# Performance work log

Hardware: AMD Instinct MI355X
Metric: run time of the kernel (lower is better)

The kernel has to match this reference:

```python
import jax, jax.numpy as jnp
import numpy as np
import math

N_HEADS = 8

def setup_inputs() -> dict:
    key = jax.random.key(0)
    ks = jax.random.split(key, 5)
    B, S, D = 2, 4096, 512
    return {
        "x": jax.random.normal(ks[0], (B, S, D), jnp.float32),
        "W_in": jax.random.normal(ks[1], (D, 3 * D), jnp.float32) * (1.0 / math.sqrt(D)),
        "b_in": jax.random.normal(ks[2], (3 * D,), jnp.float32) * 0.02,
        "W_out": jax.random.normal(ks[3], (D, D), jnp.float32) * (1.0 / math.sqrt(D)),
        "b_out": jax.random.normal(ks[4], (D,), jnp.float32) * 0.02,
        "causal_mask": 1,
    }

def reference(x, W_in, b_in, W_out, b_out, causal_mask):
    B, S, D = x.shape
    H = N_HEADS
    dh = D // H
    qkv = x @ W_in + b_in                      # [B,S,3D]
    q, k, v = jnp.split(qkv, 3, axis=-1)
    # [B,S,D] -> [B,H,S,dh]
    q = q.reshape(B, S, H, dh).transpose(0, 2, 1, 3)
    k = k.reshape(B, S, H, dh).transpose(0, 2, 1, 3)
    v = v.reshape(B, S, H, dh).transpose(0, 2, 1, 3)
    scores = jnp.einsum("bhqd,bhkd->bhqk", q, k)  # [B,H,S,S]
    if causal_mask:
        # strictly upper triangle masked to -inf (before scaling, as in torch code)
        causal = jnp.tril(jnp.ones((S, S), dtype=bool))
        scores = jnp.where(causal, scores, -jnp.inf)
    scores = scores / math.sqrt(dh)
    w = jax.nn.softmax(scores, axis=-1)
    out = jnp.einsum("bhqk,bhkd->bhqd", w, v)     # [B,H,S,dh]
    out = out.transpose(0, 2, 1, 3).reshape(B, S, D)
    return out @ W_out + b_out
```

## Files before the change

kernel.cpp:

```cpp
#include <hip/hip_runtime.h>
#include <stdint.h>

typedef __attribute__((ext_vector_type(8))) short bf16x8;
typedef __attribute__((ext_vector_type(4))) float f32x4;

__device__ __forceinline__ float bf2f(unsigned short b) {
  union { unsigned int u; float f; } c; c.u = ((unsigned int)b) << 16; return c.f;
}
__device__ __forceinline__ unsigned short f2bf(float f) {
  union { float f; unsigned int u; } c; c.f = f;
  unsigned int u = c.u;
  return (unsigned short)((u + 0x7fffu + ((u >> 16) & 1u)) >> 16);
}

__device__ __forceinline__ void gload_lds16(const void* g, void* l) {
  __builtin_amdgcn_global_load_lds((const __attribute__((address_space(1))) void*)g,
                                   (__attribute__((address_space(3))) void*)l,
                                   16, 0, 0);
}


__global__ __launch_bounds__(256) void cvt_x(const float* __restrict__ in,
                                             unsigned short* __restrict__ out, int n4) {
  int i = blockIdx.x * 256 + threadIdx.x;
  if (i < n4) {
    float4 f = ((const float4*)in)[i];
    ushort4 o;
    o.x = f2bf(f.x); o.y = f2bf(f.y); o.z = f2bf(f.z); o.w = f2bf(f.w);
    ((ushort4*)out)[i] = o;
  }
}

__global__ __launch_bounds__(256) void tw_cvt(const float* __restrict__ W,
                                              unsigned short* __restrict__ Wt, int N) {
  int idx = blockIdx.x * 256 + threadIdx.x;
  int n = idx >> 9, k = idx & 511;
  Wt[idx] = f2bf(W[(size_t)k * N + n]);
}


template<int QKV>
__global__ __launch_bounds__(256)
void gemm_bt(const unsigned short* __restrict__ A, const unsigned short* __restrict__ Bt,
             const float* __restrict__ bias, float* __restrict__ Cout,
             unsigned short* __restrict__ qo, unsigned short* __restrict__ ko,
             unsigned short* __restrict__ vo, int M, int N, int K) {
  __shared__ unsigned short As[128 * 64];
  __shared__ unsigned short Bs[128 * 64];
  const int tid = threadIdx.x;
  const int wid = tid >> 6;
  const int lane = tid & 63;
  const int row0 = blockIdx.x * 128;
  const int col0 = blockIdx.y * 128;

  f32x4 acc[4][4];
#pragma unroll
  for (int m = 0; m < 4; ++m)
#pragma unroll
    for (int n = 0; n < 4; ++n)
      acc[m][n] = (f32x4){0.f, 0.f, 0.f, 0.f};

  const int wr = (wid >> 1) * 64;
  const int wc = (wid & 1) * 64;
  const int rw = lane & 15;
  const int nk = K >> 6;

  for (int kt = 0; kt < nk; ++kt) {
    const int k0 = kt << 6;
#pragma unroll
    for (int i = 0; i < 4; ++i) {
      int c = i * 256 + tid;
      int r = c >> 3, kq = (c & 7) << 3;
      gload_lds16(A + (size_t)(row0 + r) * K + k0 + kq, As + (size_t)(i * 256 + wid * 64) * 8);
    }
#pragma unroll
    for (int i = 0; i < 4; ++i) {
      int c = i * 256 + tid;
      int r = c >> 3, kq = (c & 7) << 3;
      gload_lds16(Bt + (size_t)(col0 + r) * K + k0 + kq, Bs + (size_t)(i * 256 + wid * 64) * 8);
    }
    __syncthreads();
#pragma unroll
    for (int ks = 0; ks < 2; ++ks) {
      const int kof = ks * 32 + (lane >> 4) * 8;
      bf16x8 af[4], bfr[4];
#pragma unroll
      for (int m = 0; m < 4; ++m)
        af[m] = *(const bf16x8*)&As[(wr + m * 16 + rw) * 64 + kof];
#pragma unroll
      for (int n = 0; n < 4; ++n)
        bfr[n] = *(const bf16x8*)&Bs[(wc + n * 16 + rw) * 64 + kof];
#pragma unroll
      for (int m = 0; m < 4; ++m)
#pragma unroll
        for (int n = 0; n < 4; ++n)
          acc[m][n] = __builtin_amdgcn_mfma_f32_16x16x32_bf16(af[m], bfr[n], acc[m][n], 0, 0, 0);
    }
    __syncthreads();
  }

  const int lr4 = (lane >> 4) * 4;
  const int lc = lane & 15;
#pragma unroll
  for (int m = 0; m < 4; ++m) {
#pragma unroll
    for (int n = 0; n < 4; ++n) {
      const int col = col0 + wc + n * 16 + lc;
      const float bb = bias[col];
      const int row = row0 + wr + m * 16 + lr4;
      if (QKV) {
        const int which = col >> 9;
        const int rem = col & 511, h = rem >> 6, d = rem & 63;
        const int b = row >> 12, s = row & 4095;
        if (which == 2) {
          ushort4 u;
          u.x = f2bf(acc[m][n][0] + bb);
          u.y = f2bf(acc[m][n][1] + bb);
          u.z = f2bf(acc[m][n][2] + bb);
          u.w = f2bf(acc[m][n][3] + bb);
          *(ushort4*)&vo[(((size_t)(b * 8 + h) * 64 + d) << 12) + s] = u;
        } else {
          const float scale = (which == 0) ? 0.125f : 1.0f;
          unsigned short* dst = (which == 0) ? qo : ko;
#pragma unroll
          for (int r2 = 0; r2 < 4; ++r2)
            dst[(((size_t)(b * 8 + h) * 4096 + (s + r2)) << 6) + d] =
                f2bf((acc[m][n][r2] + bb) * scale);
        }
      } else {
#pragma unroll
        for (int r2 = 0; r2 < 4; ++r2)
          Cout[(size_t)(row + r2) * N + col] = acc[m][n][r2] + bb;
      }
    }
  }
}


__global__ __launch_bounds__(512, 2)
void attn_mfma(const unsigned short* __restrict__ Qb, const unsigned short* __restrict__ Kb,
               const unsigned short* __restrict__ Vtb, unsigned short* __restrict__ Ob,
               const int* __restrict__ causal_p) {
  __shared__ unsigned short Qs[256 * 64];
  __shared__ unsigned short Ks[64 * 64];
  __shared__ unsigned short Vs[64 * 64];
  __shared__ unsigned short Ps[8][32 * 64];

  const int tid = threadIdx.x;
  const int wid = tid >> 6;
  const int lane = tid & 63;
  const int lx = lane & 15, ly = lane >> 4, l7 = lane & 7;
  const int p = blockIdx.x;
  const int bh = blockIdx.y;
  const int causal = *causal_p;
  const int qtile = (wid < 4) ? p : (31 - p);
  const int qw = qtile * 128 + (wid & 3) * 32;
  const int qldsb = ((wid < 4) ? 0 : 128) + (wid & 3) * 32;
  const size_t qkbase = (size_t)bh * 4096 * 64;
  const size_t vbase = (size_t)bh * 64 * 4096;

  {
    const int pa = p, pb = 31 - p;
#pragma unroll
    for (int i = 0; i < 4; ++i) {
      int c = i * 512 + tid;
      int r = c >> 3, ch = c & 7;
      int qrow = (r < 128) ? (pa * 128 + r) : (pb * 128 + (r - 128));
      gload_lds16(Qb + qkbase + (size_t)qrow * 64 + ((ch ^ (r & 7)) << 3),
                  Qs + (size_t)(i * 512 + wid * 64) * 8);
    }
  }

  f32x4 o[2][4];
  float mrow[2][4], lrow[2][4];
#pragma unroll
  for (int rf = 0; rf < 2; ++rf) {
#pragma unroll
    for (int df = 0; df < 4; ++df) o[rf][df] = (f32x4){0.f, 0.f, 0.f, 0.f};
#pragma unroll
    for (int r = 0; r < 4; ++r) { mrow[rf][r] = -1e30f; lrow[rf][r] = 0.f; }
  }

  const int ktmax = causal ? (63 - 2 * p) : 63;
  for (int kt = 0; kt <= ktmax; ++kt) {
    __syncthreads();
    {
      int r = tid >> 3, ch = tid & 7;
      gload_lds16(Kb + qkbase + (size_t)(kt * 64 + r) * 64 + ((ch ^ (r & 7)) << 3),
                  Ks + (size_t)(wid * 64) * 8);
      gload_lds16(Vtb + vbase + (size_t)r * 4096 + kt * 64 + ((ch ^ (r & 7)) << 3),
                  Vs + (size_t)(wid * 64) * 8);
    }
    __syncthreads();

    const int ktb = kt * 64;
    if (!causal || ktb <= qw + 31) {
      f32x4 s[2][4];
#pragma unroll
      for (int rf = 0; rf < 2; ++rf)
#pragma unroll
        for (int cf = 0; cf < 4; ++cf) s[rf][cf] = (f32x4){0.f, 0.f, 0.f, 0.f};
#pragma unroll
      for (int ks = 0; ks < 2; ++ks) {
        const int kel = ((ks * 4 + ly) ^ l7) << 3;
        bf16x8 a[2], bb[4];
#pragma unroll
        for (int rf = 0; rf < 2; ++rf)
          a[rf] = *(const bf16x8*)&Qs[(qldsb + rf * 16 + lx) * 64 + kel];
#pragma unroll
        for (int cf = 0; cf < 4; ++cf)
          bb[cf] = *(const bf16x8*)&Ks[(cf * 16 + lx) * 64 + kel];
#pragma unroll
        for (int rf = 0; rf < 2; ++rf)
#pragma unroll
          for (int cf = 0; cf < 4; ++cf)
            s[rf][cf] = __builtin_amdgcn_mfma_f32_16x16x32_bf16(a[rf], bb[cf], s[rf][cf], 0, 0, 0);
      }

      const bool diag = causal && (ktb + 63 > qw);
#pragma unroll
      for (int rf = 0; rf < 2; ++rf) {
#pragma unroll
        for (int r = 0; r < 4; ++r) {
          const int qg = qw + rf * 16 + ly * 4 + r;
          if (diag) {
#pragma unroll
            for (int cf = 0; cf < 4; ++cf)
              if (ktb + cf * 16 + lx > qg) s[rf][cf][r] = -1e30f;
          }
          float tm = fmaxf(fmaxf(s[rf][0][r], s[rf][1][r]), fmaxf(s[rf][2][r], s[rf][3][r]));
          tm = fmaxf(tm, __shfl_xor(tm, 1));
          tm = fmaxf(tm, __shfl_xor(tm, 2));
          tm = fmaxf(tm, __shfl_xor(tm, 4));
          tm = fmaxf(tm, __shfl_xor(tm, 8));
          const float mo = mrow[rf][r];
          const float mn = fmaxf(mo, tm);
          const float scl = __expf(mo - mn);
          float ls = 0.f;
          const int ql = rf * 16 + ly * 4 + r;
          const int swz = (ql & 7) << 3;
#pragma unroll
          for (int cf = 0; cf < 4; ++cf) {
            float pv = __expf(s[rf][cf][r] - mn);
            ls += pv;
            Ps[wid][ql * 64 + ((cf * 16 + lx) ^ swz)] = f2bf(pv);
          }
          ls += __shfl_xor(ls, 1);
          ls += __shfl_xor(ls, 2);
          ls += __shfl_xor(ls, 4);
          ls += __shfl_xor(ls, 8);
          lrow[rf][r] = lrow[rf][r] * scl + ls;
          mrow[rf][r] = mn;
#pragma unroll
          for (int df = 0; df < 4; ++df) o[rf][df][r] *= scl;
        }
      }

#pragma unroll
      for (int ks = 0; ks < 2; ++ks) {
        const int kel = ((ks * 4 + ly) ^ l7) << 3;
        bf16x8 pa[2], vb_[4];
#pragma unroll
        for (int rf = 0; rf < 2; ++rf)
          pa[rf] = *(const bf16x8*)&Ps[wid][(rf * 16 + lx) * 64 + kel];
#pragma unroll
        for (int df = 0; df < 4; ++df)
          vb_[df] = *(const bf16x8*)&Vs[(df * 16 + lx) * 64 + kel];
#pragma unroll
        for (int rf = 0; rf < 2; ++rf)
#pragma unroll
          for (int df = 0; df < 4; ++df)
            o[rf][df] = __builtin_amdgcn_mfma_f32_16x16x32_bf16(pa[rf], vb_[df], o[rf][df], 0, 0, 0);
      }
    }
  }

  const int b = bh >> 3, h = bh & 7;
#pragma unroll
  for (int rf = 0; rf < 2; ++rf) {
#pragma unroll
    for (int r = 0; r < 4; ++r) {
      const float inv = 1.0f / lrow[rf][r];
      const int row = b * 4096 + qw + rf * 16 + ly * 4 + r;
#pragma unroll
      for (int df = 0; df < 4; ++df)
        Ob[(size_t)row * 512 + h * 64 + df * 16 + lx] = f2bf(o[rf][df][r] * inv);
    }
  }
}


extern "C" void kernel_launch(void* const* d_in, const int* in_sizes, int n_in,
                              void* d_out, int out_size, void* d_ws, size_t ws_size,
                              hipStream_t stream) {
  const float* x     = (const float*)d_in[0];
  const float* W_in  = (const float*)d_in[1];
  const float* b_in  = (const float*)d_in[2];
  const float* W_out = (const float*)d_in[3];
  const float* b_out = (const float*)d_in[4];
  const int* causal  = (const int*)d_in[5];
  float* out = (float*)d_out;

  unsigned short* xb   = (unsigned short*)d_ws;
  unsigned short* wint = xb + 4194304;
  unsigned short* wout = wint + 786432;
  unsigned short* qb   = wout + 262144;
  unsigned short* kb   = qb + 4194304;
  unsigned short* vt   = kb + 4194304;

  cvt_x<<<4096, 256, 0, stream>>>(x, xb, 4194304 / 4);
  tw_cvt<<<3072, 256, 0, stream>>>(W_in, wint, 1536);
  tw_cvt<<<1024, 256, 0, stream>>>(W_out, wout, 512);

  gemm_bt<1><<<dim3(64, 12), 256, 0, stream>>>(xb, wint, b_in, nullptr, qb, kb, vt,
                                               8192, 1536, 512);

  attn_mfma<<<dim3(16, 16), 512, 0, stream>>>(qb, kb, vt, xb, causal);

  gemm_bt<0><<<dim3(64, 4), 256, 0, stream>>>(xb, wout, b_out, out, nullptr, nullptr, nullptr,
                                              8192, 512, 512);
}
```

Measured before the change: 347.9 us.

## Restructure attention with double-buffered K/V, register Q, lazy softmax rescale

The attention kernel moves to 256-thread blocks, one query tile each and launched largest-first. It keeps Q fragments in registers and double-buffers K/V tiles in LDS so the next tile's load overlaps compute. Softmax now works in base 2, with log2e folded into the Q scale. It skips the max reduction and rescale when the running max stays within a threshold, and defers the row-sum shuffles to the end. Separately, the weight transpose-convert now goes through LDS tiles, and V is written row-major and then transposed by a new kernel through the output buffer, which adds a launch and extra traffic.

```diff
diff --git a/kernel.cpp b/kernel.cpp
--- a/kernel.cpp
+++ b/kernel.cpp
@@ -18,6 +18,8 @@
                                    (__attribute__((address_space(3))) void*)l,
                                    16, 0, 0);
 }
+
+#define QSCALE 0.18033688011112042f
 
 
 __global__ __launch_bounds__(256) void cvt_x(const float* __restrict__ in,
@@ -31,11 +33,44 @@
   }
 }
 
-__global__ __launch_bounds__(256) void tw_cvt(const float* __restrict__ W,
-                                              unsigned short* __restrict__ Wt, int N) {
-  int idx = blockIdx.x * 256 + threadIdx.x;
-  int n = idx >> 9, k = idx & 511;
-  Wt[idx] = f2bf(W[(size_t)k * N + n]);
+__global__ __launch_bounds__(256)
+void tw_cvt_t(const float* __restrict__ W, unsigned short* __restrict__ Wt, int N) {
+  __shared__ unsigned short T[64][68];
+  const int n0 = blockIdx.x * 64, k0 = blockIdx.y * 64;
+  const int c = threadIdx.x & 15, r = threadIdx.x >> 4;
+#pragma unroll
+  for (int i = 0; i < 4; ++i) {
+    float4 f = *(const float4*)&W[(size_t)(k0 + i * 16 + r) * N + n0 + c * 4];
+    T[c * 4 + 0][i * 16 + r] = f2bf(f.x);
+    T[c * 4 + 1][i * 16 + r] = f2bf(f.y);
+    T[c * 4 + 2][i * 16 + r] = f2bf(f.z);
+    T[c * 4 + 3][i * 16 + r] = f2bf(f.w);
+  }
+  __syncthreads();
+#pragma unroll
+  for (int i = 0; i < 4; ++i)
+    *(ushort4*)&Wt[(size_t)(n0 + i * 16 + r) * 512 + k0 + c * 4] =
+        *(const ushort4*)&T[i * 16 + r][c * 4];
+}
+
+__global__ __launch_bounds__(256)
+void vtr(const unsigned short* __restrict__ vsd, unsigned short* __restrict__ vt) {
+  __shared__ unsigned short T[64][68];
+  const int bh = blockIdx.y, s0 = blockIdx.x * 64;
+  const int c = threadIdx.x & 15, r = threadIdx.x >> 4;
+#pragma unroll
+  for (int i = 0; i < 4; ++i) {
+    ushort4 u = *(const ushort4*)&vsd[((size_t)bh * 4096 + s0 + i * 16 + r) * 64 + c * 4];
+    T[c * 4 + 0][i * 16 + r] = u.x;
+    T[c * 4 + 1][i * 16 + r] = u.y;
+    T[c * 4 + 2][i * 16 + r] = u.z;
+    T[c * 4 + 3][i * 16 + r] = u.w;
+  }
+  __syncthreads();
+#pragma unroll
+  for (int i = 0; i < 4; ++i)
+    *(ushort4*)&vt[((size_t)bh * 64 + i * 16 + r) * 4096 + s0 + c * 4] =
+        *(const ushort4*)&T[i * 16 + r][c * 4];
 }
 
 
@@ -112,21 +147,12 @@
         const int which = col >> 9;
         const int rem = col & 511, h = rem >> 6, d = rem & 63;
         const int b = row >> 12, s = row & 4095;
-        if (which == 2) {
-          ushort4 u;
-          u.x = f2bf(acc[m][n][0] + bb);
-          u.y = f2bf(acc[m][n][1] + bb);
-          u.z = f2bf(acc[m][n][2] + bb);
-          u.w = f2bf(acc[m][n][3] + bb);
-          *(ushort4*)&vo[(((size_t)(b * 8 + h) * 64 + d) << 12) + s] = u;
-        } else {
-          const float scale = (which == 0) ? 0.125f : 1.0f;
-          unsigned short* dst = (which == 0) ? qo : ko;
-#pragma unroll
-          for (int r2 = 0; r2 < 4; ++r2)
-            dst[(((size_t)(b * 8 + h) * 4096 + (s + r2)) << 6) + d] =
-                f2bf((acc[m][n][r2] + bb) * scale);
-        }
+        const float scale = (which == 0) ? QSCALE : 1.0f;
+        unsigned short* dst = (which == 0) ? qo : ((which == 1) ? ko : vo);
+#pragma unroll
+        for (int r2 = 0; r2 < 4; ++r2)
+          dst[(((size_t)(b * 8 + h) * 4096 + (s + r2)) << 6) + d] =
+              f2bf((acc[m][n][r2] + bb) * scale);
       } else {
 #pragma unroll
         for (int r2 = 0; r2 < 4; ++r2)
@@ -137,61 +163,70 @@
 }
 
 
-__global__ __launch_bounds__(512, 2)
+__global__ __launch_bounds__(256, 3)
 void attn_mfma(const unsigned short* __restrict__ Qb, const unsigned short* __restrict__ Kb,
                const unsigned short* __restrict__ Vtb, unsigned short* __restrict__ Ob,
                const int* __restrict__ causal_p) {
-  __shared__ unsigned short Qs[256 * 64];
-  __shared__ unsigned short Ks[64 * 64];
-  __shared__ unsigned short Vs[64 * 64];
-  __shared__ unsigned short Ps[8][32 * 64];
+  __shared__ unsigned short Ks[2][64 * 64];
+  __shared__ unsigned short Vs[2][64 * 64];
+  __shared__ unsigned short Ps[4][32 * 64];
 
   const int tid = threadIdx.x;
   const int wid = tid >> 6;
   const int lane = tid & 63;
   const int lx = lane & 15, ly = lane >> 4, l7 = lane & 7;
-  const int p = blockIdx.x;
+  const int p = 31 - blockIdx.x;
   const int bh = blockIdx.y;
   const int causal = *causal_p;
-  const int qtile = (wid < 4) ? p : (31 - p);
-  const int qw = qtile * 128 + (wid & 3) * 32;
-  const int qldsb = ((wid < 4) ? 0 : 128) + (wid & 3) * 32;
+  const int qw = p * 128 + wid * 32;
   const size_t qkbase = (size_t)bh * 4096 * 64;
   const size_t vbase = (size_t)bh * 64 * 4096;
 
-  {
-    const int pa = p, pb = 31 - p;
-#pragma unroll
-    for (int i = 0; i < 4; ++i) {
-      int c = i * 512 + tid;
-      int r = c >> 3, ch = c & 7;
-      int qrow = (r < 128) ? (pa * 128 + r) : (pb * 128 + (r - 128));
-      gload_lds16(Qb + qkbase + (size_t)qrow * 64 + ((ch ^ (r & 7)) << 3),
-                  Qs + (size_t)(i * 512 + wid * 64) * 8);
-    }
-  }
+  bf16x8 qf[2][2];
+#pragma unroll
+  for (int rf = 0; rf < 2; ++rf)
+#pragma unroll
+    for (int ks = 0; ks < 2; ++ks)
+      qf[rf][ks] =
+          *(const bf16x8*)(Qb + qkbase + (size_t)(qw + rf * 16 + lx) * 64 + ks * 32 + ly * 8);
 
   f32x4 o[2][4];
-  float mrow[2][4], lrow[2][4];
+  float mrow[2][4], lpart[2][4];
 #pragma unroll
   for (int rf = 0; rf < 2; ++rf) {
 #pragma unroll
     for (int df = 0; df < 4; ++df) o[rf][df] = (f32x4){0.f, 0.f, 0.f, 0.f};
 #pragma unroll
-    for (int r = 0; r < 4; ++r) { mrow[rf][r] = -1e30f; lrow[rf][r] = 0.f; }
-  }
-
-  const int ktmax = causal ? (63 - 2 * p) : 63;
+    for (int r = 0; r < 4; ++r) { mrow[rf][r] = -1e30f; lpart[rf][r] = 0.f; }
+  }
+
+  const int ktmax = causal ? (2 * p + 1) : 63;
+
+#pragma unroll
+  for (int pass = 0; pass < 2; ++pass) {
+    int c = pass * 256 + tid;
+    int r = c >> 3, ch = c & 7;
+    gload_lds16(Kb + qkbase + (size_t)r * 64 + ((ch ^ (r & 7)) << 3),
+                &Ks[0][(size_t)(pass * 256 + wid * 64) * 8]);
+    gload_lds16(Vtb + vbase + (size_t)r * 4096 + ((ch ^ (r & 7)) << 3),
+                &Vs[0][(size_t)(pass * 256 + wid * 64) * 8]);
+  }
+  __syncthreads();
+
+  int cur = 0;
   for (int kt = 0; kt <= ktmax; ++kt) {
-    __syncthreads();
-    {
-      int r = tid >> 3, ch = tid & 7;
-      gload_lds16(Kb + qkbase + (size_t)(kt * 64 + r) * 64 + ((ch ^ (r & 7)) << 3),
-                  Ks + (size_t)(wid * 64) * 8);
-      gload_lds16(Vtb + vbase + (size_t)r * 4096 + kt * 64 + ((ch ^ (r & 7)) << 3),
-                  Vs + (size_t)(wid * 64) * 8);
-    }
-    __syncthreads();
+    if (kt < ktmax) {
+      const int nx = kt + 1;
+#pragma unroll
+      for (int pass = 0; pass < 2; ++pass) {
+        int c = pass * 256 + tid;
+        int r = c >> 3, ch = c & 7;
+        gload_lds16(Kb + qkbase + (size_t)(nx * 64 + r) * 64 + ((ch ^ (r & 7)) << 3),
+                    &Ks[cur ^ 1][(size_t)(pass * 256 + wid * 64) * 8]);
+        gload_lds16(Vtb + vbase + (size_t)r * 4096 + nx * 64 + ((ch ^ (r & 7)) << 3),
+                    &Vs[cur ^ 1][(size_t)(pass * 256 + wid * 64) * 8]);
+      }
+    }
 
     const int ktb = kt * 64;
     if (!causal || ktb <= qw + 31) {
@@ -203,76 +238,104 @@
 #pragma unroll
       for (int ks = 0; ks < 2; ++ks) {
         const int kel = ((ks * 4 + ly) ^ l7) << 3;
-        bf16x8 a[2], bb[4];
+        bf16x8 kf[4];
+#pragma unroll
+        for (int cf = 0; cf < 4; ++cf)
+          kf[cf] = *(const bf16x8*)&Ks[cur][(cf * 16 + lx) * 64 + kel];
 #pragma unroll
         for (int rf = 0; rf < 2; ++rf)
-          a[rf] = *(const bf16x8*)&Qs[(qldsb + rf * 16 + lx) * 64 + kel];
-#pragma unroll
-        for (int cf = 0; cf < 4; ++cf)
-          bb[cf] = *(const bf16x8*)&Ks[(cf * 16 + lx) * 64 + kel];
-#pragma unroll
-        for (int rf = 0; rf < 2; ++rf)
 #pragma unroll
           for (int cf = 0; cf < 4; ++cf)
-            s[rf][cf] = __builtin_amdgcn_mfma_f32_16x16x32_bf16(a[rf], bb[cf], s[rf][cf], 0, 0, 0);
+            s[rf][cf] = __builtin_amdgcn_mfma_f32_16x16x32_bf16(qf[rf][ks], kf[cf], s[rf][cf], 0, 0, 0);
       }
 
       const bool diag = causal && (ktb + 63 > qw);
+      float tmx[2][4];
+      bool ok = true;
 #pragma unroll
       for (int rf = 0; rf < 2; ++rf) {
 #pragma unroll
         for (int r = 0; r < 4; ++r) {
-          const int qg = qw + rf * 16 + ly * 4 + r;
           if (diag) {
+            const int qg = qw + rf * 16 + ly * 4 + r;
 #pragma unroll
             for (int cf = 0; cf < 4; ++cf)
               if (ktb + cf * 16 + lx > qg) s[rf][cf][r] = -1e30f;
           }
-          float tm = fmaxf(fmaxf(s[rf][0][r], s[rf][1][r]), fmaxf(s[rf][2][r], s[rf][3][r]));
-          tm = fmaxf(tm, __shfl_xor(tm, 1));
-          tm = fmaxf(tm, __shfl_xor(tm, 2));
-          tm = fmaxf(tm, __shfl_xor(tm, 4));
-          tm = fmaxf(tm, __shfl_xor(tm, 8));
-          const float mo = mrow[rf][r];
-          const float mn = fmaxf(mo, tm);
-          const float scl = __expf(mo - mn);
-          float ls = 0.f;
-          const int ql = rf * 16 + ly * 4 + r;
-          const int swz = (ql & 7) << 3;
-#pragma unroll
-          for (int cf = 0; cf < 4; ++cf) {
-            float pv = __expf(s[rf][cf][r] - mn);
-            ls += pv;
-            Ps[wid][ql * 64 + ((cf * 16 + lx) ^ swz)] = f2bf(pv);
+          const float a0 = fmaxf(s[rf][0][r], s[rf][1][r]);
+          const float a1 = fmaxf(s[rf][2][r], s[rf][3][r]);
+          tmx[rf][r] = fmaxf(a0, a1);
+          ok = ok && (tmx[rf][r] <= mrow[rf][r] + 8.f);
+        }
+      }
+
+      if (__all(ok)) {
+#pragma unroll
+        for (int rf = 0; rf < 2; ++rf) {
+#pragma unroll
+          for (int r = 0; r < 4; ++r) {
+            const float mo = mrow[rf][r];
+            const int ql = rf * 16 + ly * 4 + r;
+            const int swz = (ql & 7) << 3;
+            float lp = 0.f;
+#pragma unroll
+            for (int cf = 0; cf < 4; ++cf) {
+              const float pv = __builtin_amdgcn_exp2f(s[rf][cf][r] - mo);
+              lp += pv;
+              Ps[wid][ql * 64 + ((cf * 16 + lx) ^ swz)] = f2bf(pv);
+            }
+            lpart[rf][r] += lp;
           }
-          ls += __shfl_xor(ls, 1);
-          ls += __shfl_xor(ls, 2);
-          ls += __shfl_xor(ls, 4);
-          ls += __shfl_xor(ls, 8);
-          lrow[rf][r] = lrow[rf][r] * scl + ls;
-          mrow[rf][r] = mn;
-#pragma unroll
-          for (int df = 0; df < 4; ++df) o[rf][df][r] *= scl;
+        }
+      } else {
+#pragma unroll
+        for (int rf = 0; rf < 2; ++rf) {
+#pragma unroll
+          for (int r = 0; r < 4; ++r) {
+            float tm = tmx[rf][r];
+            tm = fmaxf(tm, __shfl_xor(tm, 1));
+            tm = fmaxf(tm, __shfl_xor(tm, 2));
+            tm = fmaxf(tm, __shfl_xor(tm, 4));
+            tm = fmaxf(tm, __shfl_xor(tm, 8));
+            const float mo = mrow[rf][r];
+            const float mn = fmaxf(mo, tm);
+            const float scl = __builtin_amdgcn_exp2f(mo - mn);
+            const int ql = rf * 16 + ly * 4 + r;
+            const int swz = (ql & 7) << 3;
+            float lp = 0.f;
+#pragma unroll
+            for (int cf = 0; cf < 4; ++cf) {
+              const float pv = __builtin_amdgcn_exp2f(s[rf][cf][r] - mn);
+              lp += pv;
+              Ps[wid][ql * 64 + ((cf * 16 + lx) ^ swz)] = f2bf(pv);
+            }
+            lpart[rf][r] = lpart[rf][r] * scl + lp;
+            mrow[rf][r] = mn;
+#pragma unroll
+            for (int df = 0; df < 4; ++df) o[rf][df][r] *= scl;
+          }
         }
       }
 
 #pragma unroll
       for (int ks = 0; ks < 2; ++ks) {
         const int kel = ((ks * 4 + ly) ^ l7) << 3;
-        bf16x8 pa[2], vb_[4];
+        bf16x8 pa[2], vf[4];
 #pragma unroll
         for (int rf = 0; rf < 2; ++rf)
           pa[rf] = *(const bf16x8*)&Ps[wid][(rf * 16 + lx) * 64 + kel];
 #pragma unroll
         for (int df = 0; df < 4; ++df)
-          vb_[df] = *(const bf16x8*)&Vs[(df * 16 + lx) * 64 + kel];
+          vf[df] = *(const bf16x8*)&Vs[cur][(df * 16 + lx) * 64 + kel];
 #pragma unroll
         for (int rf = 0; rf < 2; ++rf)
 #pragma unroll
           for (int df = 0; df < 4; ++df)
-            o[rf][df] = __builtin_amdgcn_mfma_f32_16x16x32_bf16(pa[rf], vb_[df], o[rf][df], 0, 0, 0);
-      }
-    }
+            o[rf][df] = __builtin_amdgcn_mfma_f32_16x16x32_bf16(pa[rf], vf[df], o[rf][df], 0, 0, 0);
+      }
+    }
+    __syncthreads();
+    cur ^= 1;
   }
 
   const int b = bh >> 3, h = bh & 7;
@@ -280,7 +343,12 @@
   for (int rf = 0; rf < 2; ++rf) {
 #pragma unroll
     for (int r = 0; r < 4; ++r) {
-      const float inv = 1.0f / lrow[rf][r];
+      float l = lpart[rf][r];
+      l += __shfl_xor(l, 1);
+      l += __shfl_xor(l, 2);
+      l += __shfl_xor(l, 4);
+      l += __shfl_xor(l, 8);
+      const float inv = 1.0f / l;
       const int row = b * 4096 + qw + rf * 16 + ly * 4 + r;
 #pragma unroll
       for (int df = 0; df < 4; ++df)
@@ -307,15 +375,18 @@
   unsigned short* qb   = wout + 262144;
   unsigned short* kb   = qb + 4194304;
   unsigned short* vt   = kb + 4194304;
-
-  cvt_x<<<4096, 256, 0, stream>>>(x, xb, 4194304 / 4);
-  tw_cvt<<<3072, 256, 0, stream>>>(W_in, wint, 1536);
-  tw_cvt<<<1024, 256, 0, stream>>>(W_out, wout, 512);
-
-  gemm_bt<1><<<dim3(64, 12), 256, 0, stream>>>(xb, wint, b_in, nullptr, qb, kb, vt,
+  unsigned short* vsd  = (unsigned short*)d_out;
+
+  cvt_x<<<4096, 256, 0, stream>>>(x, xb, 1048576);
+  tw_cvt_t<<<dim3(24, 8), 256, 0, stream>>>(W_in, wint, 1536);
+  tw_cvt_t<<<dim3(8, 8), 256, 0, stream>>>(W_out, wout, 512);
+
+  gemm_bt<1><<<dim3(64, 12), 256, 0, stream>>>(xb, wint, b_in, nullptr, qb, kb, vsd,
                                                8192, 1536, 512);
 
-  attn_mfma<<<dim3(16, 16), 512, 0, stream>>>(qb, kb, vt, xb, causal);
+  vtr<<<dim3(64, 16), 256, 0, stream>>>(vsd, vt);
+
+  attn_mfma<<<dim3(32, 16), 256, 0, stream>>>(qb, kb, vt, xb, causal);
 
   gemm_bt<0><<<dim3(64, 4), 256, 0, stream>>>(xb, wout, b_out, out, nullptr, nullptr, nullptr,
                                               8192, 512, 512);
```

Measured after the change: 385.2 us. 10.7% more time.
